# Kernel tuning notes

Hardware: AMD Instinct MI355X
Metric: run time of the kernel (lower is better)

Reference implementation:

```python
import jax, jax.numpy as jnp
import numpy as np

TARGET_SPARSITY = 0.9
LN_EPS = 1e-5


def ternary_quant(W):
    """BitNet-b1.58 style ternary quantization: W -> {-1,0,+1} * mean(|W|).
    Straight-through estimator so gradients pass to the latent weights."""
    scale = jnp.mean(jnp.abs(W))
    q = jnp.clip(jnp.round(W / (scale + 1e-8)), -1.0, 1.0) * scale
    return W + jax.lax.stop_gradient(q - W)


def layernorm(x, gamma, beta):
    mu = jnp.mean(x, axis=-1, keepdims=True)
    var = jnp.var(x, axis=-1, keepdims=True)
    return (x - mu) * jax.lax.rsqrt(var + LN_EPS) * gamma + beta


def setup_inputs() -> dict:
    key = jax.random.key(0)
    ks = jax.random.split(key, 3)
    B, S, D, N = 4, 2048, 2048, 8192
    x = jax.random.normal(ks[0], (B, S, D), dtype=jnp.float32)
    W_syn = jax.random.normal(ks[1], (N, D), dtype=jnp.float32) * (1.0 / np.sqrt(D))
    b_syn = jnp.zeros((N,), dtype=jnp.float32)
    W_out = jax.random.normal(ks[2], (D, N), dtype=jnp.float32) * (1.0 / np.sqrt(N))
    b_out = jnp.zeros((D,), dtype=jnp.float32)
    gamma = jnp.ones((D,), dtype=jnp.float32)
    beta = jnp.zeros((D,), dtype=jnp.float32)
    return {"x": x, "W_syn": W_syn, "b_syn": b_syn, "W_out": W_out,
            "b_out": b_out, "gamma": gamma, "beta": beta}


def reference(x, W_syn, b_syn, W_out, b_out, gamma, beta):
    B, S, D = x.shape
    N = W_syn.shape[0]
    x_flat = x.reshape(-1, D)  # [T, D], T = B*S

    # RNU: ternary-weight synapses + sparse firing (keep top (1-sparsity) per token)
    z = x_flat @ ternary_quant(W_syn).T + b_syn  # [T, N]
    k = max(1, int(N * (1.0 - TARGET_SPARSITY)))
    topv, _ = jax.lax.top_k(z, k)                 # [T, k]
    thresh = topv[:, -1:]                          # k-th largest per token
    hidden = jnp.where(z >= thresh, jax.nn.relu(z), 0.0)  # sparse firing rates

    # Ternary output projection
    out = hidden @ ternary_quant(W_out).T + b_out  # [T, D]
    out = out.reshape(B, S, D)

    # Residual + LayerNorm
    return layernorm(x + out, gamma, beta)
```

## Files before the change

kernel.cpp:

```cpp
#include <hip/hip_runtime.h>


typedef __attribute__((ext_vector_type(8))) short short8;
typedef __attribute__((ext_vector_type(4))) float f32x4;

__device__ __forceinline__ float bf2f(unsigned h) {
    return __uint_as_float(h << 16);
}
__device__ __forceinline__ unsigned f2bf(float f) {
    unsigned u = __float_as_uint(f);
    return (u + 0x7fffu + ((u >> 16) & 1u)) >> 16;
}

typedef __attribute__((address_space(1))) const void gq_void;
typedef __attribute__((address_space(3))) void ls_void;
__device__ __forceinline__ void gload16(const void* g, void* l) {
    __builtin_amdgcn_global_load_lds((gq_void*)g, (ls_void*)l, 16, 0, 0);
}

__global__ __launch_bounds__(64) void init_detect(float* sc, const unsigned* g_raw,
                                                  int* flag) {
    if (threadIdx.x < 16) sc[threadIdx.x] = 0.0f;
    if (threadIdx.x == 0) *flag = (g_raw[0] == 0x3F803F80u) ? 1 : 0;
}

__global__ __launch_bounds__(256) void split_x(const void* __restrict__ src,
                                               unsigned short* __restrict__ hi,
                                               unsigned short* __restrict__ lo, int n,
                                               const int* __restrict__ flagp) {
    const int flag = *flagp;
    int idx = blockIdx.x * 256 + threadIdx.x;
    int stride = gridDim.x * 256;
    if (flag) {
        const uint4* s = (const uint4*)src;
        uint4* dh = (uint4*)hi;
        uint4* dl = (uint4*)lo;
        uint4 zz; zz.x = zz.y = zz.z = zz.w = 0u;
        for (int i = idx; i < n / 8; i += stride) { dh[i] = s[i]; dl[i] = zz; }
    } else {
        const float4* s = (const float4*)src;
        uint2* dh = (uint2*)hi;
        uint2* dl = (uint2*)lo;
        for (int i = idx; i < n / 4; i += stride) {
            float4 v = s[i];
            unsigned h0 = f2bf(v.x), h1 = f2bf(v.y), h2 = f2bf(v.z), h3 = f2bf(v.w);
            unsigned l0 = f2bf(v.x - bf2f(h0));
            unsigned l1 = f2bf(v.y - bf2f(h1));
            unsigned l2 = f2bf(v.z - bf2f(h2));
            unsigned l3 = f2bf(v.w - bf2f(h3));
            uint2 oh; oh.x = h0 | (h1 << 16); oh.y = h2 | (h3 << 16);
            uint2 ol; ol.x = l0 | (l1 << 16); ol.y = l2 | (l3 << 16);
            dh[i] = oh;
            dl[i] = ol;
        }
    }
}

__global__ __launch_bounds__(256) void to_f32(const void* __restrict__ src,
                                              float* __restrict__ dst, int n,
                                              const int* __restrict__ flagp) {
    const int flag = *flagp;
    int i = blockIdx.x * 256 + threadIdx.x;
    if (i >= n) return;
    if (flag) dst[i] = bf2f((unsigned)((const unsigned short*)src)[i]);
    else dst[i] = ((const float*)src)[i];
}

__global__ __launch_bounds__(256) void abs_sum_any(const void* __restrict__ w, int n,
                                                   float* __restrict__ out,
                                                   const int* __restrict__ flagp) {
    const int flag = *flagp;
    int idx = blockIdx.x * 256 + threadIdx.x;
    int stride = gridDim.x * 256;
    float s = 0.0f;
    if (flag) {
        const uint4* wv = (const uint4*)w;
        for (int c = idx; c < n / 8; c += stride) {
            uint4 v = wv[c];
            unsigned a[4] = {v.x, v.y, v.z, v.w};
#pragma unroll
            for (int j = 0; j < 4; j++)
                s += fabsf(bf2f(a[j] & 0xffffu)) + fabsf(bf2f(a[j] >> 16));
        }
    } else {
        const float4* wv = (const float4*)w;
        for (int c = idx; c < n / 4; c += stride) {
            float4 v = wv[c];
            s += fabsf(v.x) + fabsf(v.y) + fabsf(v.z) + fabsf(v.w);
        }
    }
#pragma unroll
    for (int off = 32; off; off >>= 1) s += __shfl_down(s, off);
    __shared__ float red[4];
    int lane = threadIdx.x & 63, wv_id = threadIdx.x >> 6;
    if (lane == 0) red[wv_id] = s;
    __syncthreads();
    if (threadIdx.x == 0) atomicAdd(out, red[0] + red[1] + red[2] + red[3]);
}

__global__ __launch_bounds__(64) void finalize_scale(float* sc, float inv_count) {
    if (threadIdx.x == 0) {
        sc[2] = sc[0] * inv_count;
        sc[3] = sc[1] * inv_count;
    }
}

__global__ __launch_bounds__(256) void quantize_any(const void* __restrict__ w,
                                                    unsigned short* __restrict__ q,
                                                    const float* __restrict__ sc, int idx,
                                                    int n, const int* __restrict__ flagp) {
    const int flag = *flagp;
    const float d = sc[idx] + 1e-8f;
    int i = blockIdx.x * 256 + threadIdx.x;
    int stride = gridDim.x * 256;
    if (flag) {
        const uint4* wv = (const uint4*)w;
        uint4* qv = (uint4*)q;
        for (; i < n / 8; i += stride) {
            uint4 v = wv[i];
            unsigned a[4] = {v.x, v.y, v.z, v.w};
            unsigned r[4];
#pragma unroll
            for (int j = 0; j < 4; j++) {
                float lo = bf2f(a[j] & 0xffffu);
                float hi = bf2f(a[j] >> 16);
                float rl = fminf(1.0f, fmaxf(-1.0f, rintf(lo / d)));
                float rh = fminf(1.0f, fmaxf(-1.0f, rintf(hi / d)));
                r[j] = f2bf(rl) | (f2bf(rh) << 16);
            }
            uint4 o;
            o.x = r[0]; o.y = r[1]; o.z = r[2]; o.w = r[3];
            qv[i] = o;
        }
    } else {
        const float4* wv = (const float4*)w;
        uint2* qv = (uint2*)q;
        for (; i < n / 4; i += stride) {
            float4 v = wv[i];
            float r0 = fminf(1.0f, fmaxf(-1.0f, rintf(v.x / d)));
            float r1 = fminf(1.0f, fmaxf(-1.0f, rintf(v.y / d)));
            float r2 = fminf(1.0f, fmaxf(-1.0f, rintf(v.z / d)));
            float r3 = fminf(1.0f, fmaxf(-1.0f, rintf(v.w / d)));
            uint2 o;
            o.x = f2bf(r0) | (f2bf(r1) << 16);
            o.y = f2bf(r2) | (f2bf(r3) << 16);
            qv[i] = o;
        }
    }
}

template <int BM, int BN, bool TWO>
__global__ __launch_bounds__(256) void gemm_bt_t(const unsigned short* __restrict__ A0,
                                                 const unsigned short* __restrict__ A1,
                                                 const unsigned short* __restrict__ B,
                                                 float* __restrict__ C,
                                                 const float* __restrict__ biasf,
                                                 const float* __restrict__ scp, int scidx,
                                                 int N, int K) {
    constexpr int WM = BM / 2;
    constexpr int WN = BN / 2;
    constexpr int AM = WM / 16;
    constexpr int AN = WN / 16;
    __shared__ uint4 sA[BM * 8];
    __shared__ uint4 sL[TWO ? BM * 8 : 4];
    __shared__ uint4 sB[BN * 8];
    const int tid = threadIdx.x;
    const int lane = tid & 63;
    const int wave = tid >> 6;
    const int wm = (wave >> 1) * WM;
    const int wn = (wave & 1) * WN;
    const int m0 = blockIdx.y * BM;
    const int n0 = blockIdx.x * BN;
    const int l15 = lane & 15;
    const int quad = lane >> 4;

    f32x4 acc[AM][AN];
#pragma unroll
    for (int i = 0; i < AM; i++)
#pragma unroll
        for (int j = 0; j < AN; j++) acc[i][j] = (f32x4){0.f, 0.f, 0.f, 0.f};

    const unsigned short* Abase = A0 + (size_t)m0 * K;
    const unsigned short* Lbase = TWO ? (A1 + (size_t)m0 * K) : nullptr;
    const unsigned short* Bbase = B + (size_t)n0 * K;

    for (int k0 = 0; k0 < K; k0 += 64) {
#pragma unroll
        for (int i = 0; i < BM * 8 / 256; i++) {
            int s = tid + i * 256;
            int r = s >> 3, c = s & 7;
            size_t go = (size_t)r * K + k0 + c * 8;
            gload16(Abase + go, sA + i * 256 + wave * 64);
            if (TWO) gload16(Lbase + go, sL + i * 256 + wave * 64);
        }
#pragma unroll
        for (int i = 0; i < BN * 8 / 256; i++) {
            int s = tid + i * 256;
            int r = s >> 3, c = s & 7;
            size_t go = (size_t)r * K + k0 + c * 8;
            gload16(Bbase + go, sB + i * 256 + wave * 64);
        }
        __syncthreads();
#pragma unroll
        for (int kk = 0; kk < 64; kk += 32) {
            const int jj = (kk >> 3) + quad;
            short8 ah[AM], bfr[AN];
#pragma unroll
            for (int t = 0; t < AM; t++)
                ah[t] = *(const short8*)&sA[(wm + t * 16 + l15) * 8 + jj];
#pragma unroll
            for (int t = 0; t < AN; t++)
                bfr[t] = *(const short8*)&sB[(wn + t * 16 + l15) * 8 + jj];
#pragma unroll
            for (int im = 0; im < AM; im++)
#pragma unroll
                for (int in = 0; in < AN; in++)
                    acc[im][in] = __builtin_amdgcn_mfma_f32_16x16x32_bf16(
                        ah[im], bfr[in], acc[im][in], 0, 0, 0);
            if (TWO) {
                short8 al[AM];
#pragma unroll
                for (int t = 0; t < AM; t++)
                    al[t] = *(const short8*)&sL[(wm + t * 16 + l15) * 8 + jj];
#pragma unroll
                for (int im = 0; im < AM; im++)
#pragma unroll
                    for (int in = 0; in < AN; in++)
                        acc[im][in] = __builtin_amdgcn_mfma_f32_16x16x32_bf16(
                            al[im], bfr[in], acc[im][in], 0, 0, 0);
            }
        }
        __syncthreads();
    }

    float scale = scp[scidx];
#pragma unroll
    for (int in = 0; in < AN; in++) {
        int col = n0 + wn + in * 16 + l15;
        float bv = biasf[col];
#pragma unroll
        for (int im = 0; im < AM; im++) {
            int rbase = m0 + wm + im * 16 + quad * 4;
#pragma unroll
            for (int r = 0; r < 4; r++) {
                C[(size_t)(rbase + r) * N + col] = scale * acc[im][in][r] + bv;
            }
        }
    }
}

__global__ __launch_bounds__(256) void topk_hidden(const float* __restrict__ z,
                                                   unsigned short* __restrict__ hidden,
                                                   int N, int k) {
    __shared__ unsigned keys[8192];
    __shared__ unsigned hist[2048];
    __shared__ unsigned csum[256];
    __shared__ unsigned sh_want, sh_kk;
    const int tid = threadIdx.x;
    const size_t row = blockIdx.x;
    const float* zr = z + row * (size_t)N;

    for (int i = tid; i < N; i += 256) {
        unsigned u = __float_as_uint(zr[i]);
        keys[i] = (u & 0x80000000u) ? ~u : (u | 0x80000000u);
    }
    if (tid == 0) { sh_want = 0u; sh_kk = (unsigned)k; }
    __syncthreads();

    for (int p = 0; p < 3; p++) {
        const int shift = (p == 0) ? 21 : (p == 1) ? 10 : 0;
        const int bits = (p == 2) ? 10 : 11;
        const int nb = 1 << bits;
        const unsigned want = sh_want;
        const unsigned kk = sh_kk;
        const int hs = shift + bits;
        for (int b = tid; b < nb; b += 256) hist[b] = 0u;
        __syncthreads();
        for (int i = tid; i < N; i += 256) {
            unsigned u = keys[i];
            bool match = (hs >= 32) ? true : ((u >> hs) == (want >> hs));
            if (match) atomicAdd(&hist[(u >> shift) & (nb - 1)], 1u);
        }
        __syncthreads();
        const int cs = nb >> 8;
        unsigned cv = 0;
        for (int j = 0; j < cs; j++) cv += hist[tid * cs + j];
        csum[tid] = cv;
        __syncthreads();
        for (int off = 1; off < 256; off <<= 1) {
            unsigned add = (tid + off < 256) ? csum[tid + off] : 0u;
            __syncthreads();
            csum[tid] += add;
            __syncthreads();
        }
        unsigned excl = (tid < 255) ? csum[tid + 1] : 0u;
        if (excl < kk && kk <= csum[tid]) {
            unsigned running = excl;
            for (int b = tid * cs + cs - 1; b >= tid * cs; b--) {
                unsigned h = hist[b];
                if (running + h >= kk) {
                    sh_want = want | ((unsigned)b << shift);
                    sh_kk = kk - running;
                    break;
                }
                running += h;
            }
        }
        __syncthreads();
    }

    const unsigned kth = sh_want;
    unsigned short* hr = hidden + row * (size_t)N;
    for (int i = tid; i < N; i += 256) {
        unsigned u = keys[i];
        float f = (u & 0x80000000u) ? __uint_as_float(u & 0x7fffffffu)
                                    : __uint_as_float(~u);
        float h = (u >= kth) ? fmaxf(f, 0.0f) : 0.0f;
        hr[i] = (unsigned short)f2bf(h);
    }
}

__global__ __launch_bounds__(256) void ln_kernel(const unsigned short* __restrict__ xh,
                                                 const unsigned short* __restrict__ xl,
                                                 const float* __restrict__ o,
                                                 const float* __restrict__ gamma,
                                                 const float* __restrict__ beta,
                                                 float* __restrict__ y, int D) {
    const int tid = threadIdx.x;
    const size_t row = blockIdx.x;
    const unsigned short* xhr = xh + row * (size_t)D;
    const unsigned short* xlr = xl + row * (size_t)D;
    const float* orow = o + row * (size_t)D;
    float v[8];
    float s = 0.0f, s2 = 0.0f;
#pragma unroll
    for (int j = 0; j < 8; j++) {
        int i = tid + j * 256;
        float val = bf2f((unsigned)xhr[i]) + bf2f((unsigned)xlr[i]) + orow[i];
        v[j] = val;
        s += val;
        s2 += val * val;
    }
#pragma unroll
    for (int off = 32; off; off >>= 1) {
        s += __shfl_down(s, off);
        s2 += __shfl_down(s2, off);
    }
    __shared__ float red[8];
    int lane = tid & 63, wv = tid >> 6;
    if (lane == 0) { red[wv] = s; red[4 + wv] = s2; }
    __syncthreads();
    float S = red[0] + red[1] + red[2] + red[3];
    float S2 = red[4] + red[5] + red[6] + red[7];
    float mu = S / (float)D;
    float var = S2 / (float)D - mu * mu;
    float inv = rsqrtf(var + 1e-5f);
#pragma unroll
    for (int j = 0; j < 8; j++) {
        int i = tid + j * 256;
        y[row * (size_t)D + i] = (v[j] - mu) * inv * gamma[i] + beta[i];
    }
}

extern "C" void kernel_launch(void* const* d_in, const int* in_sizes, int n_in,
                              void* d_out, int out_size, void* d_ws, size_t ws_size,
                              hipStream_t stream) {
    const void* x_raw = d_in[0];
    const void* Wsyn_raw = d_in[1];
    const void* bsyn_raw = d_in[2];
    const void* Wout_raw = d_in[3];
    const void* bout_raw = d_in[4];
    const void* gamma_raw = d_in[5];
    const void* beta_raw = d_in[6];
    float* out = (float*)d_out;

    const int M = 8192, D = 2048, N = 8192, K1 = 2048;
    const int kTop = 819;
    const int NW = M * D;

    char* wsb = (char*)d_ws;
    float* sc = (float*)wsb;
    int* flag = (int*)(wsb + 128);
    float* gamma_f = (float*)(wsb + 4096);
    float* beta_f = (float*)(wsb + 12288);
    float* bout_f = (float*)(wsb + 20480);
    float* bsyn_f = (float*)(wsb + 28672);
    unsigned short* x_hi = (unsigned short*)(wsb + 65536);
    unsigned short* x_lo = (unsigned short*)(wsb + 65536 + 1ull * 33554432ull);
    unsigned short* qsyn = (unsigned short*)(wsb + 65536 + 2ull * 33554432ull);
    unsigned short* qout = (unsigned short*)(wsb + 65536 + 3ull * 33554432ull);
    const size_t FIXED = 65536 + 4ull * 33554432ull;

    const size_t per_row = (size_t)N * 4 + (size_t)N * 2;
    size_t avail = (ws_size > FIXED) ? ws_size - FIXED : 0;
    long mc = (long)(avail / per_row);
    mc &= ~127L;
    if (mc > M) mc = M;
    if (mc < 128) mc = 128;
    const int Mc = (int)mc;
    char* chunk_base = wsb + FIXED;

    init_detect<<<1, 64, 0, stream>>>(sc, (const unsigned*)gamma_raw, flag);

    split_x<<<2048, 256, 0, stream>>>(x_raw, x_hi, x_lo, M * D, flag);
    to_f32<<<(N + 255) / 256, 256, 0, stream>>>(bsyn_raw, bsyn_f, N, flag);
    to_f32<<<(D + 255) / 256, 256, 0, stream>>>(bout_raw, bout_f, D, flag);
    to_f32<<<(D + 255) / 256, 256, 0, stream>>>(gamma_raw, gamma_f, D, flag);
    to_f32<<<(D + 255) / 256, 256, 0, stream>>>(beta_raw, beta_f, D, flag);

    abs_sum_any<<<2048, 256, 0, stream>>>(Wsyn_raw, NW, sc + 0, flag);
    abs_sum_any<<<2048, 256, 0, stream>>>(Wout_raw, NW, sc + 1, flag);
    finalize_scale<<<1, 64, 0, stream>>>(sc, 1.0f / 16777216.0f);
    quantize_any<<<2048, 256, 0, stream>>>(Wsyn_raw, qsyn, sc, 2, NW, flag);
    quantize_any<<<2048, 256, 0, stream>>>(Wout_raw, qout, sc, 3, NW, flag);

    for (int m0 = 0; m0 < M; m0 += Mc) {
        const int rows = (M - m0 < Mc) ? (M - m0) : Mc;
        float* z = (float*)chunk_base;
        unsigned short* hidden = (unsigned short*)(chunk_base + (size_t)Mc * N * 4);
        float* outf = (float*)chunk_base;

        dim3 g1(N / 128, rows / 128);
        gemm_bt_t<128, 128, true><<<g1, 256, 0, stream>>>(
            x_hi + (size_t)m0 * K1, x_lo + (size_t)m0 * K1, qsyn, z, bsyn_f, sc, 2, N,
            K1);

        topk_hidden<<<rows, 256, 0, stream>>>(z, hidden, N, kTop);

        dim3 g2(D / 64, rows / 128);
        gemm_bt_t<128, 64, false><<<g2, 256, 0, stream>>>(hidden, nullptr, qout, outf,
                                                          bout_f, sc, 3, D, N);

        ln_kernel<<<rows, 256, 0, stream>>>(x_hi + (size_t)m0 * D, x_lo + (size_t)m0 * D,
                                            outf, gamma_f, beta_f, out + (size_t)m0 * D,
                                            D);
    }
}
```

Measured before the change: 1.875 ms.

## Replace first GEMM with 256x256 tile, 8-wave ping-pong pipelined MFMA kernel

Adds a new 512-thread GEMM kernel with 256x256 output tiles, double-buffered LDS staging through direct global-to-LDS loads, XOR-swizzled LDS layout, and workgroup-id remapping for L2 locality. It interleaves MFMA phases with the next tile's loads, using barriers and s_setprio so loads overlap compute. The x@Wsyn GEMM, with hi/lo split of x, now uses this kernel, and the chunk size is rounded to multiples of 256 rows to match. Risks include register pressure from 32 accumulators per thread and many barriers per K step.

```diff
diff --git a/kernel.cpp b/kernel.cpp
--- a/kernel.cpp
+++ b/kernel.cpp
@@ -17,6 +17,14 @@
 __device__ __forceinline__ void gload16(const void* g, void* l) {
     __builtin_amdgcn_global_load_lds((gq_void*)g, (ls_void*)l, 16, 0, 0);
 }
+
+#define CFENCE() asm volatile("" ::: "memory")
+#define BARRIER()                    \
+    do {                             \
+        CFENCE();                    \
+        __builtin_amdgcn_s_barrier(); \
+        CFENCE();                    \
+    } while (0)
 
 __global__ __launch_bounds__(64) void init_detect(float* sc, const unsigned* g_raw,
                                                   int* flag) {
@@ -149,6 +157,164 @@
     }
 }
 
+template <bool DUAL_A>
+__global__ __launch_bounds__(512, 2) void gemm8p(const unsigned short* __restrict__ A0,
+                                                 const unsigned short* __restrict__ A1,
+                                                 const unsigned short* __restrict__ B,
+                                                 float* __restrict__ C,
+                                                 const float* __restrict__ biasf,
+                                                 const float* __restrict__ scp,
+                                                 int scidx, int N, int K) {
+    __shared__ uint4 L4[8192];
+
+    const int tid = threadIdx.x;
+    const int lane = tid & 63;
+    const int wave = tid >> 6;
+    const int wr = wave >> 2;
+    const int wc = wave & 3;
+    const int l15 = lane & 15;
+    const int quad = lane >> 4;
+
+    const int nwg = gridDim.x * gridDim.y;
+    int orig = blockIdx.y * gridDim.x + blockIdx.x;
+    int id = orig;
+    if ((nwg & 7) == 0) id = (orig & 7) * (nwg >> 3) + (orig >> 3);
+    const int bx = id % gridDim.x;
+    const int by = id / gridDim.x;
+    const int m0 = by * 256;
+    const int n0 = bx * 256;
+
+    f32x4 acc[8][4];
+#pragma unroll
+    for (int i = 0; i < 8; i++)
+#pragma unroll
+        for (int j = 0; j < 4; j++) acc[i][j] = (f32x4){0.f, 0.f, 0.f, 0.f};
+
+    const unsigned short* Apan0 = A0 + (size_t)m0 * K;
+    const unsigned short* Apan1 = DUAL_A ? (A1 + (size_t)m0 * K) : nullptr;
+    const unsigned short* Bpan = B + (size_t)n0 * K;
+
+    const int NT = DUAL_A ? (K >> 5) : (K >> 6);
+
+    auto stage = [&](const unsigned short* g, int kcol, int dstChunkBase) {
+#pragma unroll
+        for (int i = 0; i < 2; i++) {
+            int pc = tid + i * 512;
+            int r = pc >> 2;
+            int c4 = (pc & 3) ^ (r & 3);
+            gload16(g + (size_t)r * K + kcol + c4 * 8,
+                    L4 + dstChunkBase + (tid & 448) + i * 512);
+        }
+    };
+    auto dstA = [&](int b, int s) { return (b * 2 + s) * 1024; };
+    auto dstB = [&](int b, int s) { return 4096 + (b * 2 + s) * 1024; };
+
+    auto rdA = [&](int b, int s, int R) -> short8 {
+        return *(const short8*)(L4 + (b * 2 + s) * 1024 + R * 4 + (quad ^ (R & 3)));
+    };
+    auto rdB = [&](int b, int s, int R) -> short8 {
+        return *(const short8*)(L4 + 4096 + (b * 2 + s) * 1024 + R * 4 +
+                                (quad ^ (R & 3)));
+    };
+
+    stage(Apan0, 0, dstA(0, 0));
+    stage(Bpan, 0, dstB(0, 0));
+    stage(Apan0, 32, dstA(0, 1));
+    stage(Bpan, 32, dstB(0, 1));
+    asm volatile("s_waitcnt vmcnt(4)" ::: "memory");
+    BARRIER();
+
+    for (int t = 0; t < NT; ++t) {
+        const int b = t & 1;
+        const int bn = b ^ 1;
+        const bool st = (t + 1 < NT);
+        const unsigned short* Anext =
+            (DUAL_A && ((t + 1) & 1)) ? Apan1 : Apan0;
+        const int kbn = DUAL_A ? (((t + 1) >> 1) << 6) : ((t + 1) << 6);
+
+        short8 a[8], b0, b1;
+
+#pragma unroll
+        for (int m = 0; m < 8; m++) a[m] = rdA(b, 0, wr * 128 + m * 16 + l15);
+        b0 = rdB(b, 0, wc * 64 + 0 + l15);
+        b1 = rdB(b, 0, wc * 64 + 16 + l15);
+        if (st) stage(Anext, kbn + 0, dstA(bn, 0));
+        BARRIER();
+        __builtin_amdgcn_s_setprio(1);
+#pragma unroll
+        for (int m = 0; m < 8; m++) {
+            acc[m][0] = __builtin_amdgcn_mfma_f32_16x16x32_bf16(a[m], b0, acc[m][0], 0, 0, 0);
+            acc[m][1] = __builtin_amdgcn_mfma_f32_16x16x32_bf16(a[m], b1, acc[m][1], 0, 0, 0);
+        }
+        __builtin_amdgcn_s_setprio(0);
+        BARRIER();
+
+        b0 = rdB(b, 0, wc * 64 + 32 + l15);
+        b1 = rdB(b, 0, wc * 64 + 48 + l15);
+        if (st) {
+            stage(Bpan, kbn + 0, dstB(bn, 0));
+            asm volatile("s_waitcnt vmcnt(4)" ::: "memory");
+        } else {
+            asm volatile("s_waitcnt vmcnt(0)" ::: "memory");
+        }
+        BARRIER();
+        __builtin_amdgcn_s_setprio(1);
+#pragma unroll
+        for (int m = 0; m < 8; m++) {
+            acc[m][2] = __builtin_amdgcn_mfma_f32_16x16x32_bf16(a[m], b0, acc[m][2], 0, 0, 0);
+            acc[m][3] = __builtin_amdgcn_mfma_f32_16x16x32_bf16(a[m], b1, acc[m][3], 0, 0, 0);
+        }
+        __builtin_amdgcn_s_setprio(0);
+        BARRIER();
+
+#pragma unroll
+        for (int m = 0; m < 8; m++) a[m] = rdA(b, 1, wr * 128 + m * 16 + l15);
+        b0 = rdB(b, 1, wc * 64 + 0 + l15);
+        b1 = rdB(b, 1, wc * 64 + 16 + l15);
+        if (st) stage(Anext, kbn + 32, dstA(bn, 1));
+        BARRIER();
+        __builtin_amdgcn_s_setprio(1);
+#pragma unroll
+        for (int m = 0; m < 8; m++) {
+            acc[m][0] = __builtin_amdgcn_mfma_f32_16x16x32_bf16(a[m], b0, acc[m][0], 0, 0, 0);
+            acc[m][1] = __builtin_amdgcn_mfma_f32_16x16x32_bf16(a[m], b1, acc[m][1], 0, 0, 0);
+        }
+        __builtin_amdgcn_s_setprio(0);
+        BARRIER();
+
+        b0 = rdB(b, 1, wc * 64 + 32 + l15);
+        b1 = rdB(b, 1, wc * 64 + 48 + l15);
+        if (st) {
+            stage(Bpan, kbn + 32, dstB(bn, 1));
+            asm volatile("s_waitcnt vmcnt(4)" ::: "memory");
+        }
+        BARRIER();
+        __builtin_amdgcn_s_setprio(1);
+#pragma unroll
+        for (int m = 0; m < 8; m++) {
+            acc[m][2] = __builtin_amdgcn_mfma_f32_16x16x32_bf16(a[m], b0, acc[m][2], 0, 0, 0);
+            acc[m][3] = __builtin_amdgcn_mfma_f32_16x16x32_bf16(a[m], b1, acc[m][3], 0, 0, 0);
+        }
+        __builtin_amdgcn_s_setprio(0);
+        BARRIER();
+    }
+
+    const float scale = scp[scidx];
+#pragma unroll
+    for (int n = 0; n < 4; n++) {
+        int col = n0 + wc * 64 + n * 16 + l15;
+        float bv = biasf[col];
+#pragma unroll
+        for (int m = 0; m < 8; m++) {
+            int rbase = m0 + wr * 128 + m * 16 + quad * 4;
+#pragma unroll
+            for (int r = 0; r < 4; r++) {
+                C[(size_t)(rbase + r) * N + col] = scale * acc[m][n][r] + bv;
+            }
+        }
+    }
+}
+
 template <int BM, int BN, bool TWO>
 __global__ __launch_bounds__(256) void gemm_bt_t(const unsigned short* __restrict__ A0,
                                                  const unsigned short* __restrict__ A1,
@@ -394,9 +560,9 @@
     const size_t per_row = (size_t)N * 4 + (size_t)N * 2;
     size_t avail = (ws_size > FIXED) ? ws_size - FIXED : 0;
     long mc = (long)(avail / per_row);
-    mc &= ~127L;
+    mc &= ~255L;
     if (mc > M) mc = M;
-    if (mc < 128) mc = 128;
+    if (mc < 256) mc = 256;
     const int Mc = (int)mc;
     char* chunk_base = wsb + FIXED;
 
@@ -420,10 +586,10 @@
         unsigned short* hidden = (unsigned short*)(chunk_base + (size_t)Mc * N * 4);
         float* outf = (float*)chunk_base;
 
-        dim3 g1(N / 128, rows / 128);
-        gemm_bt_t<128, 128, true><<<g1, 256, 0, stream>>>(
-            x_hi + (size_t)m0 * K1, x_lo + (size_t)m0 * K1, qsyn, z, bsyn_f, sc, 2, N,
-            K1);
+        dim3 g1(N / 256, rows / 256);
+        gemm8p<true><<<g1, 512, 0, stream>>>(x_hi + (size_t)m0 * K1,
+                                             x_lo + (size_t)m0 * K1, qsyn, z, bsyn_f,
+                                             sc, 2, N, K1);
 
         topk_hidden<<<rows, 256, 0, stream>>>(z, hidden, N, kTop);
 
```

After: 2.047 ms. 1.09x slower.
